# Kernel tuning notes

Hardware: AMD Instinct MI355X
Metric: run time of the kernel (lower is better)

The kernel has to match this reference:

```python
import jax, jax.numpy as jnp
import numpy as np

SEQ, BATCH, IN_F, STATE, OUT_F = 2048, 32, 256, 512, 256


def setup_inputs() -> dict:
    key = jax.random.key(0)
    k1, k2, k3, k4 = jax.random.split(key, 4)
    x = jax.random.normal(k1, (SEQ, BATCH, IN_F), dtype=jnp.float32)
    # lambda_log init per module __init__ with rmin=0, rmax=1:
    # u ~ U(0,1); lambda_log = log(-0.5*log(u*(rmax+rmin)*(rmax-rmin)+rmin^2)) = log(-0.5*log(u))
    u = jax.random.uniform(k2, (STATE,), dtype=jnp.float32, minval=1e-6, maxval=1.0)
    lambda_log = jnp.log(-0.5 * jnp.log(u))
    B = jax.random.normal(k3, (STATE, IN_F), dtype=jnp.float32) / np.float32(np.sqrt(IN_F))
    C = jax.random.normal(k4, (OUT_F, STATE), dtype=jnp.float32) / np.float32(np.sqrt(STATE))
    return {"input": x, "lambda_log": lambda_log, "B": B, "C": C}


def reference(input, lambda_log, B, C):
    # mode='sequential', inner_loops=1, rnn_burnin=0, done=None, hidden=None
    lamda = jnp.exp(-jnp.exp(lambda_log))                 # [N]
    gamma = jnp.sqrt(1.0 - lamda * lamda + 1e-7)          # [N]
    # project all timesteps at once: b_seq[s,b,n] = gamma_n * (x_s @ B^T)
    b_seq = jnp.einsum('sbi,ni->sbn', input, B) * gamma   # [S,B,N]

    def step(state, b_t):
        new_state = lamda * state + b_t                   # diagonal LRU recurrence
        return new_state, new_state

    init = jnp.zeros((input.shape[1], lambda_log.shape[0]), dtype=input.dtype)
    final_state, states = jax.lax.scan(step, init, b_seq)  # states: [S,B,N]
    output = jnp.einsum('sbn,on->sbo', states, C)          # [S,B,O]
    return output, final_state
```

## Files before the change

kernel.cpp:

```cpp
#include <hip/hip_runtime.h>

#define SEQ   2048
#define BATCH 32
#define INF   256
#define NST   512
#define OUTF  256
#define CLEN  32
#define NCH   64
#define NJOB  4
#define NCG   (NCH / NJOB)
#define NBLK  (NCG * BATCH)

typedef __bf16 bf16;
typedef __bf16 bf16x8 __attribute__((ext_vector_type(8)));
typedef float  f32x4  __attribute__((ext_vector_type(4)));
typedef unsigned long long ull;

__global__ void k_prep(const float* __restrict__ ll,
                       const float* __restrict__ Bm,
                       const float* __restrict__ Cm,
                       float* __restrict__ lam,
                       float* __restrict__ lamG,
                       float* __restrict__ l2la,
                       bf16* __restrict__ Bb,
                       bf16* __restrict__ Cb) {
  int i = blockIdx.x * 256 + threadIdx.x;
  if (i < NST) {
    float e = expf(ll[i]);
    float lmb = expf(-e);
    lam[i] = lmb;
    l2la[i] = -e * 1.44269504088896341f;
    float p = lmb;
#pragma unroll
    for (int q = 0; q < 7; ++q) p *= p;
    lamG[i] = p;
  }
  if (i < NST * INF) {
    int n = i >> 8;
    float lmb = expf(-expf(ll[n]));
    float g = sqrtf(1.0f - lmb * lmb + 1e-7f);
    Bb[i] = (bf16)(Bm[i] * g);
  }
  if (i < OUTF * NST) {
    Cb[i] = (bf16)(Cm[i]);
  }
}

__device__ __forceinline__ void xload(const float* __restrict__ xp, int tid,
                                      float4 xr[4]) {
#pragma unroll
  for (int rep = 0; rep < 4; ++rep) {
    int slot = rep * 512 + tid;
    int row = slot >> 6, col4 = slot & 63;
    xr[rep] = *(const float4*)(xp + (size_t)row * (BATCH * INF) + col4 * 4);
  }
}

__device__ __forceinline__ void xstore(char* xsb, int tid, const float4 xr[4]) {
#pragma unroll
  for (int rep = 0; rep < 4; ++rep) {
    int slot = rep * 512 + tid;
    int row = slot >> 6, col4 = slot & 63;
    union { bf16 h[4]; ull u; } pk;
    pk.h[0] = (bf16)xr[rep].x; pk.h[1] = (bf16)xr[rep].y;
    pk.h[2] = (bf16)xr[rep].z; pk.h[3] = (bf16)xr[rep].w;
    int byte = (row * (INF * 2) + col4 * 8) ^ ((row & 15) << 4);
    *(ull*)(xsb + byte) = pk.u;
  }
}

__device__ __forceinline__ void reg_scan(f32x4 acc[2][4], float carry[4],
                                         const float la[4], const float l4[4],
                                         int kg, int rl) {
#pragma unroll
  for (int mt = 0; mt < 2; ++mt) {
    float sl[4][4];
#pragma unroll
    for (int nt = 0; nt < 4; ++nt) {
      sl[nt][0] = acc[mt][nt][0];
      sl[nt][1] = fmaf(la[nt], sl[nt][0], acc[mt][nt][1]);
      sl[nt][2] = fmaf(la[nt], sl[nt][1], acc[mt][nt][2]);
      sl[nt][3] = fmaf(la[nt], sl[nt][2], acc[mt][nt][3]);
    }
    float G[4];
#pragma unroll
    for (int nt = 0; nt < 4; ++nt) {
      float g1 = __shfl_up(sl[nt][3], 16);
      G[nt] = (kg >= 1) ? fmaf(l4[nt], g1, sl[nt][3]) : sl[nt][3];
    }
#pragma unroll
    for (int nt = 0; nt < 4; ++nt) {
      float l8 = l4[nt] * l4[nt];
      float g2 = __shfl_up(G[nt], 32);
      G[nt] = (kg >= 2) ? fmaf(l8, g2, G[nt]) : G[nt];
    }
#pragma unroll
    for (int nt = 0; nt < 4; ++nt) {
      float X = __shfl_up(G[nt], 16);
      X = (kg >= 1) ? X : 0.0f;
      float l8 = l4[nt] * l4[nt];
      float p4k = ((kg & 1) ? l4[nt] : 1.0f) * ((kg & 2) ? l8 : 1.0f);
      float cin = fmaf(p4k, carry[nt], X);
      float l2 = la[nt] * la[nt], l3 = l2 * la[nt];
      acc[mt][nt][0] = fmaf(la[nt], cin, sl[nt][0]);
      acc[mt][nt][1] = fmaf(l2, cin, sl[nt][1]);
      acc[mt][nt][2] = fmaf(l3, cin, sl[nt][2]);
      acc[mt][nt][3] = fmaf(l4[nt], cin, sl[nt][3]);
    }
#pragma unroll
    for (int nt = 0; nt < 4; ++nt)
      carry[nt] = __shfl(acc[mt][nt][3], rl + 48);
  }
}

__device__ __forceinline__ void gemm1_l2(const char* xsb, const bf16* __restrict__ Bb,
                                         f32x4 acc[2][4], int n0, int rl, int kg) {
#pragma unroll
  for (int k = 0; k < 8; ++k) {
    bf16x8 af[2], bfr[4];
#pragma unroll
    for (int mt = 0; mt < 2; ++mt) {
      int row = mt * 16 + rl;
      int byte = (row * (INF * 2) + (k * 32 + kg * 8) * 2) ^ (rl << 4);
      af[mt] = *(const bf16x8*)(xsb + byte);
    }
#pragma unroll
    for (int nt = 0; nt < 4; ++nt)
      bfr[nt] = *(const bf16x8*)(Bb + (size_t)(n0 + nt * 16 + rl) * INF + k * 32 + kg * 8);
#pragma unroll
    for (int mt = 0; mt < 2; ++mt)
#pragma unroll
      for (int nt = 0; nt < 4; ++nt)
        acc[mt][nt] = __builtin_amdgcn_mfma_f32_16x16x32_bf16(af[mt], bfr[nt], acc[mt][nt], 0, 0, 0);
  }
}

__global__ __launch_bounds__(512, 2)
void k_pass0f(const float* __restrict__ x, const bf16* __restrict__ Bb,
              const float* __restrict__ lam, float* __restrict__ Z,
              ull* __restrict__ bfrag) {
  __shared__ __align__(16) char xs[4][CLEN * INF * 2];

  const int tid = threadIdx.x, wid = tid >> 6, lane = tid & 63;
  const int rl = lane & 15, kg = lane >> 4;
  const int b = blockIdx.x >> 4, cg = blockIdx.x & 15;
  const int n0 = wid * 64;

  float la[4], l4[4], carry[4];
#pragma unroll
  for (int nt = 0; nt < 4; ++nt) {
    float v = lam[n0 + nt * 16 + rl];
    la[nt] = v; l4[nt] = (v * v) * (v * v);
    carry[nt] = 0.0f;
  }

  bf16x8 Breg[8][4];
#pragma unroll
  for (int k = 0; k < 8; ++k)
#pragma unroll
    for (int nt = 0; nt < 4; ++nt)
      Breg[k][nt] = *(const bf16x8*)(Bb + (size_t)(n0 + nt * 16 + rl) * INF + k * 32 + kg * 8);

  {
    float4 xr[4];
    xload(x + ((size_t)(cg * NJOB * CLEN) * BATCH + b) * INF, tid, xr);
    xstore(xs[0], tid, xr);
    xload(x + ((size_t)((cg * NJOB + 1) * CLEN) * BATCH + b) * INF, tid, xr);
    xstore(xs[1], tid, xr);
  }
  __syncthreads();

#pragma unroll
  for (int jj = 0; jj < NJOB; ++jj) {
    const int c = cg * NJOB + jj;
    f32x4 acc[2][4] = {};
#pragma unroll
    for (int k = 0; k < 8; ++k) {
      bf16x8 af[2];
#pragma unroll
      for (int mt = 0; mt < 2; ++mt) {
        int row = mt * 16 + rl;
        int byte = (row * (INF * 2) + (k * 32 + kg * 8) * 2) ^ (rl << 4);
        af[mt] = *(const bf16x8*)(&xs[jj][0] + byte);
      }
#pragma unroll
      for (int mt = 0; mt < 2; ++mt)
#pragma unroll
        for (int nt = 0; nt < 4; ++nt)
          acc[mt][nt] = __builtin_amdgcn_mfma_f32_16x16x32_bf16(af[mt], Breg[k][nt], acc[mt][nt], 0, 0, 0);
    }

    float4 xr[4];
    if (jj < 2)
      xload(x + ((size_t)((c + 2) * CLEN) * BATCH + b) * INF, tid, xr);

    reg_scan(acc, carry, la, l4, kg, rl);

    if (jj < 2) {
      xstore(xs[jj + 2], tid, xr);
      __syncthreads();
    }

    {
      ull* dst = bfrag + ((size_t)(((cg * BATCH + b) * NJOB + jj) * 8 + wid)) * 512 + lane;
#pragma unroll
      for (int mt = 0; mt < 2; ++mt)
#pragma unroll
        for (int nt = 0; nt < 4; ++nt) {
          union { bf16 h[4]; ull u; } pk;
          pk.h[0] = (bf16)acc[mt][nt][0];
          pk.h[1] = (bf16)acc[mt][nt][1];
          pk.h[2] = (bf16)acc[mt][nt][2];
          pk.h[3] = (bf16)acc[mt][nt][3];
          dst[(mt * 4 + nt) * 64] = pk.u;
        }
    }

    if (jj == NJOB - 1) {
      if (kg == 0)
#pragma unroll
        for (int nt = 0; nt < 4; ++nt)
          Z[((size_t)cg * BATCH + b) * NST + n0 + nt * 16 + rl] = carry[nt];
    }
  }
}

__global__ __launch_bounds__(128)
void k_chain(const float* __restrict__ Z, const float* __restrict__ lamG,
             float* __restrict__ S0, float* __restrict__ fin) {
  const int b = blockIdx.x;
  const int n = blockIdx.y * 128 + threadIdx.x;
  const float lG = lamG[n];
  float z[NCG];
#pragma unroll
  for (int g = 0; g < NCG; ++g)
    z[g] = Z[((size_t)g * BATCH + b) * NST + n];
  float s = 0.0f;
#pragma unroll
  for (int g = 0; g < NCG; ++g) {
    S0[((size_t)g * BATCH + b) * NST + n] = s;
    s = fmaf(lG, s, z[g]);
  }
  fin[(size_t)b * NST + n] = s;
}

__global__ __launch_bounds__(512)
void k_gemm2d(const ull* __restrict__ bfrag, const bf16* __restrict__ Cb,
              const float* __restrict__ S0, const float* __restrict__ l2la,
              float* __restrict__ out) {
  __shared__ __align__(16) char ss[32 * NST * 2];

  const int tid = threadIdx.x, wid = tid >> 6, lane = tid & 63;
  const int rl = lane & 15, kg = lane >> 4;
  const int c = blockIdx.x >> 5, b = blockIdx.x & 31;
  const int cg = c >> 2, jj = c & 3;

  const ull* src8 = bfrag + ((size_t)((cg * BATCH + b) * NJOB + jj)) * 4096;
  const float* S0g = S0 + ((size_t)cg * BATCH + b) * NST;
#pragma unroll
  for (int q = 0; q < 8; ++q) {
    int chunk = q * 512 + tid;
    int widx = chunk >> 9;
    int fr = (chunk >> 6) & 7;
    int mt = fr >> 2, nt = fr & 3;
    int ls = chunk & 63;
    int kgs = ls >> 4, rls = ls & 15;
    int n = widx * 64 + nt * 16 + rls;
    int t0 = mt * 16 + kgs * 4;
    int dt0 = jj * 32 + t0;

    union { ull u; bf16 h[4]; } in;
    in.u = src8[chunk];
    float l2 = l2la[n];
    float s0 = S0g[n];
    float e = exp2f((float)(dt0 + 1) * l2);
    float lm = exp2f(l2);
#pragma unroll
    for (int r = 0; r < 4; ++r) {
      float s = fmaf(e, s0, (float)in.h[r]);
      int t = t0 + r;
      int byte = (t * (NST * 2) + n * 2) ^ ((t & 15) << 4);
      *(bf16*)(&ss[0] + byte) = (bf16)s;
      e *= lm;
    }
  }
  __syncthreads();

  const int o0 = wid * 32;
  f32x4 acc[2][2] = {};
  bf16x8 cf[2];
#pragma unroll
  for (int ot2 = 0; ot2 < 2; ++ot2)
    cf[ot2] = *(const bf16x8*)(Cb + (size_t)(o0 + ot2 * 16 + rl) * NST + kg * 8);
#pragma unroll
  for (int kq = 0; kq < 16; ++kq) {
    const int k0 = kq * 32;
    bf16x8 cfn[2];
    if (kq < 15)
#pragma unroll
      for (int ot2 = 0; ot2 < 2; ++ot2)
        cfn[ot2] = *(const bf16x8*)(Cb + (size_t)(o0 + ot2 * 16 + rl) * NST + k0 + 32 + kg * 8);
    bf16x8 af[2];
#pragma unroll
    for (int mf = 0; mf < 2; ++mf) {
      int t = mf * 16 + rl;
      af[mf] = *(const bf16x8*)(&ss[0] +
          ((t * (NST * 2) + (k0 + kg * 8) * 2) ^ ((t & 15) << 4)));
    }
#pragma unroll
    for (int mf = 0; mf < 2; ++mf)
#pragma unroll
      for (int ot2 = 0; ot2 < 2; ++ot2)
        acc[mf][ot2] = __builtin_amdgcn_mfma_f32_16x16x32_bf16(af[mf], cf[ot2], acc[mf][ot2], 0, 0, 0);
    if (kq < 15) {
      cf[0] = cfn[0]; cf[1] = cfn[1];
    }
  }

#pragma unroll
  for (int mf = 0; mf < 2; ++mf)
#pragma unroll
    for (int ot2 = 0; ot2 < 2; ++ot2)
#pragma unroll
      for (int r = 0; r < 4; ++r) {
        int ml = mf * 16 + kg * 4 + r;
        size_t srow = (size_t)c * 32 + ml;
        int o = o0 + ot2 * 16 + rl;
        out[(srow * BATCH + b) * OUTF + o] = acc[mf][ot2][r];
      }
}

__global__ __launch_bounds__(512, 2)
void k_pass0_fb(const float* __restrict__ x, const bf16* __restrict__ Bb,
                const float* __restrict__ lam, float* __restrict__ Z) {
  __shared__ __align__(16) char xs[2][CLEN * INF * 2];

  const int tid = threadIdx.x, wid = tid >> 6, lane = tid & 63;
  const int rl = lane & 15, kg = lane >> 4;
  const int b = blockIdx.x >> 4, cg = blockIdx.x & 15;
  const int n0 = wid * 64;

  float la[4], l4[4], carry[4];
#pragma unroll
  for (int nt = 0; nt < 4; ++nt) {
    float v = lam[n0 + nt * 16 + rl];
    la[nt] = v; l4[nt] = (v * v) * (v * v);
    carry[nt] = 0.0f;
  }

  bf16x8 Breg[8][4];
#pragma unroll
  for (int k = 0; k < 8; ++k)
#pragma unroll
    for (int nt = 0; nt < 4; ++nt)
      Breg[k][nt] = *(const bf16x8*)(Bb + (size_t)(n0 + nt * 16 + rl) * INF + k * 32 + kg * 8);

  {
    float4 xr0[4];
    xload(x + ((size_t)(cg * NJOB * CLEN) * BATCH + b) * INF, tid, xr0);
    xstore(xs[0], tid, xr0);
  }
  __syncthreads();

#pragma unroll
  for (int jj = 0; jj < NJOB; ++jj) {
    const int c = cg * NJOB + jj;
    f32x4 acc[2][4] = {};
#pragma unroll
    for (int k = 0; k < 8; ++k) {
      bf16x8 af[2];
#pragma unroll
      for (int mt = 0; mt < 2; ++mt) {
        int row = mt * 16 + rl;
        int byte = (row * (INF * 2) + (k * 32 + kg * 8) * 2) ^ (rl << 4);
        af[mt] = *(const bf16x8*)(&xs[jj & 1][0] + byte);
      }
#pragma unroll
      for (int mt = 0; mt < 2; ++mt)
#pragma unroll
        for (int nt = 0; nt < 4; ++nt)
          acc[mt][nt] = __builtin_amdgcn_mfma_f32_16x16x32_bf16(af[mt], Breg[k][nt], acc[mt][nt], 0, 0, 0);
    }

    if (jj < NJOB - 1) {
      float4 xr[4];
      xload(x + ((size_t)((c + 1) * CLEN) * BATCH + b) * INF, tid, xr);
      reg_scan(acc, carry, la, l4, kg, rl);
      xstore(xs[(jj + 1) & 1], tid, xr);
      __syncthreads();
    } else {
      reg_scan(acc, carry, la, l4, kg, rl);
      if (kg == 0)
#pragma unroll
        for (int nt = 0; nt < 4; ++nt)
          Z[((size_t)cg * BATCH + b) * NST + n0 + nt * 16 + rl] = carry[nt];
    }
  }
}

__global__ __launch_bounds__(512)
void k_pass1_fb(const float* __restrict__ x, const bf16* __restrict__ Bb,
                const bf16* __restrict__ Cb, const float* __restrict__ lam,
                const float* __restrict__ S0, float* __restrict__ out,
                float* __restrict__ fin) {
  __shared__ __align__(16) char xs[2][CLEN * INF * 2];
  __shared__ __align__(16) char ss[CLEN * NST * 2];

  const int tid = threadIdx.x, wid = tid >> 6, lane = tid & 63;
  const int rl = lane & 15, kg = lane >> 4;
  const int b = blockIdx.x >> 4, cg = blockIdx.x & 15;
  const int n0 = wid * 64;

  float la[4], l4[4], carry[4];
#pragma unroll
  for (int nt = 0; nt < 4; ++nt) {
    float v = lam[n0 + nt * 16 + rl];
    la[nt] = v; l4[nt] = (v * v) * (v * v);
    carry[nt] = S0[((size_t)cg * BATCH + b) * NST + n0 + nt * 16 + rl];
  }
  {
    float4 xr0[4];
    xload(x + ((size_t)(cg * NJOB * CLEN) * BATCH + b) * INF, tid, xr0);
    xstore(xs[0], tid, xr0);
  }
  __syncthreads();

#pragma unroll
  for (int jj = 0; jj < NJOB; ++jj) {
    const int c = cg * NJOB + jj;
    f32x4 acc[2][4] = {};
    gemm1_l2(&xs[jj & 1][0], Bb, acc, n0, rl, kg);
    {
      float4 xr[4];
      const int lastj = (jj == NJOB - 1);
      if (!lastj)
        xload(x + ((size_t)((c + 1) * CLEN) * BATCH + b) * INF, tid, xr);
      reg_scan(acc, carry, la, l4, kg, rl);
      if (c == NCH - 1 && kg == 0)
#pragma unroll
        for (int nt = 0; nt < 4; ++nt)
          fin[(size_t)b * NST + n0 + nt * 16 + rl] = carry[nt];
      __syncthreads();
#pragma unroll
      for (int mt = 0; mt < 2; ++mt)
#pragma unroll
        for (int nt = 0; nt < 4; ++nt)
#pragma unroll
          for (int r = 0; r < 4; ++r) {
            int t = mt * 16 + kg * 4 + r;
            int n = n0 + nt * 16 + rl;
            int byte = (t * (NST * 2) + n * 2) ^ ((t & 15) << 4);
            *(bf16*)(&ss[0] + byte) = (bf16)acc[mt][nt][r];
          }
      if (!lastj) xstore(xs[(jj + 1) & 1], tid, xr);
    }
    __syncthreads();

    const int o0 = wid * 32;
    f32x4 a2[2][2] = {};
#pragma unroll
    for (int k0 = 0; k0 < NST; k0 += 32) {
      bf16x8 af[2], cf[2];
#pragma unroll
      for (int mt = 0; mt < 2; ++mt) {
        int t = mt * 16 + rl;
        int byte = (t * (NST * 2) + (k0 + kg * 8) * 2) ^ (rl << 4);
        af[mt] = *(const bf16x8*)(&ss[0] + byte);
      }
#pragma unroll
      for (int ot = 0; ot < 2; ++ot)
        cf[ot] = *(const bf16x8*)(Cb + (size_t)(o0 + ot * 16 + rl) * NST + k0 + kg * 8);
#pragma unroll
      for (int mt = 0; mt < 2; ++mt)
#pragma unroll
        for (int ot = 0; ot < 2; ++ot)
          a2[mt][ot] = __builtin_amdgcn_mfma_f32_16x16x32_bf16(af[mt], cf[ot], a2[mt][ot], 0, 0, 0);
    }
#pragma unroll
    for (int mt = 0; mt < 2; ++mt)
#pragma unroll
      for (int ot = 0; ot < 2; ++ot)
#pragma unroll
        for (int r = 0; r < 4; ++r) {
          int t = mt * 16 + kg * 4 + r;
          int o = o0 + ot * 16 + rl;
          out[(((size_t)(c * CLEN + t)) * BATCH + b) * OUTF + o] = a2[mt][ot][r];
        }
  }
}

extern "C" void kernel_launch(void* const* d_in, const int* in_sizes, int n_in,
                              void* d_out, int out_size, void* d_ws, size_t ws_size,
                              hipStream_t stream) {
  const float* x  = (const float*)d_in[0];
  const float* ll = (const float*)d_in[1];
  const float* Bm = (const float*)d_in[2];
  const float* Cm = (const float*)d_in[3];

  char* ws = (char*)d_ws;
  float* lam  = (float*)(ws);
  float* lamG = (float*)(ws + 2048);
  float* l2la = (float*)(ws + 4096);
  bf16*  Bb   = (bf16*)(ws + 6144);
  bf16*  Cb   = (bf16*)(ws + 6144 + NST * INF * 2);
  float* Z    = (float*)(ws + 6144 + NST * INF * 2 + OUTF * NST * 2);
  float* S0   = (float*)((char*)Z + (size_t)NCG * BATCH * NST * 4);
  ull*   bfrag= (ull*)((char*)S0 + (size_t)NCG * BATCH * NST * 4);
  const size_t NEED = ((char*)bfrag - ws) + (size_t)SEQ * BATCH * NST * 2;

  float* out = (float*)d_out;
  float* fin = out + (size_t)SEQ * BATCH * OUTF;

  k_prep<<<dim3(512), dim3(256), 0, stream>>>(ll, Bm, Cm, lam, lamG, l2la, Bb, Cb);
  if (ws_size >= NEED) {
    k_pass0f<<<dim3(NBLK), dim3(512), 0, stream>>>(x, Bb, lam, Z, bfrag);
    k_chain<<<dim3(BATCH, 4), dim3(128), 0, stream>>>(Z, lamG, S0, fin);
    k_gemm2d<<<dim3(2048), dim3(512), 0, stream>>>(bfrag, Cb, S0, l2la, out);
  } else {
    k_pass0_fb<<<dim3(NBLK), dim3(512), 0, stream>>>(x, Bb, lam, Z);
    k_chain<<<dim3(BATCH, 4), dim3(128), 0, stream>>>(Z, lamG, S0, fin);
    k_pass1_fb<<<dim3(NBLK), dim3(512), 0, stream>>>(x, Bb, Cb, lam, S0, out, fin);
  }
}
```

Before: 121.2 us.

## Store intermediate scan in row-major layout and use precomputed lambda power table

The first pass now writes its bf16 intermediate states in a plain time-by-state row-major layout instead of MFMA fragment order, so the second GEMM kernel can load them with 16-byte vector reads. The per-element exp2 for the carry correction is replaced by a 128-row table of lambda powers built in the prep kernel. The GEMM kernel now handles 64 timesteps per block (half as many blocks) to get more reuse of the C fragments. The cost is scattered 2-byte stores in pass0, a serial 128-iteration loop in the prep kernel, extra table reads, and doubled shared memory per block.

```diff
diff --git a/kernel.cpp b/kernel.cpp
--- a/kernel.cpp
+++ b/kernel.cpp
@@ -21,7 +21,7 @@
                        const float* __restrict__ Cm,
                        float* __restrict__ lam,
                        float* __restrict__ lamG,
-                       float* __restrict__ l2la,
+                       float* __restrict__ Lam32,
                        bf16* __restrict__ Bb,
                        bf16* __restrict__ Cb) {
   int i = blockIdx.x * 256 + threadIdx.x;
@@ -29,11 +29,15 @@
     float e = expf(ll[i]);
     float lmb = expf(-e);
     lam[i] = lmb;
-    l2la[i] = -e * 1.44269504088896341f;
     float p = lmb;
 #pragma unroll
     for (int q = 0; q < 7; ++q) p *= p;
     lamG[i] = p;
+    float ee = lmb;
+    for (int dt = 0; dt < 128; ++dt) {
+      Lam32[(size_t)dt * NST + i] = ee;
+      ee *= lmb;
+    }
   }
   if (i < NST * INF) {
     int n = i >> 8;
@@ -136,9 +140,9 @@
 }
 
 __global__ __launch_bounds__(512, 2)
-void k_pass0f(const float* __restrict__ x, const bf16* __restrict__ Bb,
-              const float* __restrict__ lam, float* __restrict__ Z,
-              ull* __restrict__ bfrag) {
+void k_pass0tn(const float* __restrict__ x, const bf16* __restrict__ Bb,
+               const float* __restrict__ lam, float* __restrict__ Z,
+               bf16* __restrict__ bfrag) {
   __shared__ __align__(16) char xs[4][CLEN * INF * 2];
 
   const int tid = threadIdx.x, wid = tid >> 6, lane = tid & 63;
@@ -202,18 +206,17 @@
     }
 
     {
-      ull* dst = bfrag + ((size_t)(((cg * BATCH + b) * NJOB + jj) * 8 + wid)) * 512 + lane;
+      bf16* dstp = bfrag + (((size_t)cg * BATCH + b) * 128 + jj * 32) * NST;
 #pragma unroll
       for (int mt = 0; mt < 2; ++mt)
 #pragma unroll
-        for (int nt = 0; nt < 4; ++nt) {
-          union { bf16 h[4]; ull u; } pk;
-          pk.h[0] = (bf16)acc[mt][nt][0];
-          pk.h[1] = (bf16)acc[mt][nt][1];
-          pk.h[2] = (bf16)acc[mt][nt][2];
-          pk.h[3] = (bf16)acc[mt][nt][3];
-          dst[(mt * 4 + nt) * 64] = pk.u;
-        }
+        for (int nt = 0; nt < 4; ++nt)
+#pragma unroll
+          for (int r = 0; r < 4; ++r) {
+            int t = mt * 16 + kg * 4 + r;
+            int n = n0 + nt * 16 + rl;
+            dstp[(size_t)t * NST + n] = (bf16)acc[mt][nt][r];
+          }
     }
 
     if (jj == NJOB - 1) {
@@ -245,49 +248,46 @@
 }
 
 __global__ __launch_bounds__(512)
-void k_gemm2d(const ull* __restrict__ bfrag, const bf16* __restrict__ Cb,
-              const float* __restrict__ S0, const float* __restrict__ l2la,
+void k_gemm2e(const bf16* __restrict__ bfrag, const bf16* __restrict__ Cb,
+              const float* __restrict__ S0, const float* __restrict__ Lam32,
               float* __restrict__ out) {
-  __shared__ __align__(16) char ss[32 * NST * 2];
+  __shared__ __align__(16) char ss[64 * NST * 2];
 
   const int tid = threadIdx.x, wid = tid >> 6, lane = tid & 63;
   const int rl = lane & 15, kg = lane >> 4;
-  const int c = blockIdx.x >> 5, b = blockIdx.x & 31;
-  const int cg = c >> 2, jj = c & 3;
-
-  const ull* src8 = bfrag + ((size_t)((cg * BATCH + b) * NJOB + jj)) * 4096;
-  const float* S0g = S0 + ((size_t)cg * BATCH + b) * NST;
+  const int c2 = blockIdx.x >> 5, b = blockIdx.x & 31;
+  const int cg = c2 >> 1;
+  const int dtbase = (c2 & 1) * 64;
+
+  const int n8 = (tid & 63) * 8;
+  float s0g[8];
+#pragma unroll
+  for (int j = 0; j < 8; ++j)
+    s0g[j] = S0[((size_t)cg * BATCH + b) * NST + n8 + j];
+
+  const uint4* src = (const uint4*)(bfrag +
+      (((size_t)cg * BATCH + b) * 128 + dtbase) * NST);
 #pragma unroll
   for (int q = 0; q < 8; ++q) {
     int chunk = q * 512 + tid;
-    int widx = chunk >> 9;
-    int fr = (chunk >> 6) & 7;
-    int mt = fr >> 2, nt = fr & 3;
-    int ls = chunk & 63;
-    int kgs = ls >> 4, rls = ls & 15;
-    int n = widx * 64 + nt * 16 + rls;
-    int t0 = mt * 16 + kgs * 4;
-    int dt0 = jj * 32 + t0;
-
-    union { ull u; bf16 h[4]; } in;
-    in.u = src8[chunk];
-    float l2 = l2la[n];
-    float s0 = S0g[n];
-    float e = exp2f((float)(dt0 + 1) * l2);
-    float lm = exp2f(l2);
-#pragma unroll
-    for (int r = 0; r < 4; ++r) {
-      float s = fmaf(e, s0, (float)in.h[r]);
-      int t = t0 + r;
-      int byte = (t * (NST * 2) + n * 2) ^ ((t & 15) << 4);
-      *(bf16*)(&ss[0] + byte) = (bf16)s;
-      e *= lm;
-    }
+    int tl = chunk >> 6;
+    union { uint4 u; bf16 h[8]; } in, ot;
+    in.u = src[chunk];
+    const float4* lp = (const float4*)(Lam32 + (size_t)(dtbase + tl) * NST + n8);
+    float4 L0 = lp[0], L1 = lp[1];
+    float lv[8] = {L0.x, L0.y, L0.z, L0.w, L1.x, L1.y, L1.z, L1.w};
+#pragma unroll
+    for (int j = 0; j < 8; ++j) {
+      float s = fmaf(lv[j], s0g[j], (float)in.h[j]);
+      ot.h[j] = (bf16)s;
+    }
+    int byte = (tl * (NST * 2) + (chunk & 63) * 16) ^ ((tl & 15) << 4);
+    *(uint4*)(&ss[0] + byte) = ot.u;
   }
   __syncthreads();
 
   const int o0 = wid * 32;
-  f32x4 acc[2][2] = {};
+  f32x4 acc[4][2] = {};
   bf16x8 cf[2];
 #pragma unroll
   for (int ot2 = 0; ot2 < 2; ++ot2)
@@ -300,15 +300,15 @@
 #pragma unroll
       for (int ot2 = 0; ot2 < 2; ++ot2)
         cfn[ot2] = *(const bf16x8*)(Cb + (size_t)(o0 + ot2 * 16 + rl) * NST + k0 + 32 + kg * 8);
-    bf16x8 af[2];
-#pragma unroll
-    for (int mf = 0; mf < 2; ++mf) {
+    bf16x8 af[4];
+#pragma unroll
+    for (int mf = 0; mf < 4; ++mf) {
       int t = mf * 16 + rl;
       af[mf] = *(const bf16x8*)(&ss[0] +
           ((t * (NST * 2) + (k0 + kg * 8) * 2) ^ ((t & 15) << 4)));
     }
 #pragma unroll
-    for (int mf = 0; mf < 2; ++mf)
+    for (int mf = 0; mf < 4; ++mf)
 #pragma unroll
       for (int ot2 = 0; ot2 < 2; ++ot2)
         acc[mf][ot2] = __builtin_amdgcn_mfma_f32_16x16x32_bf16(af[mf], cf[ot2], acc[mf][ot2], 0, 0, 0);
@@ -318,13 +318,13 @@
   }
 
 #pragma unroll
-  for (int mf = 0; mf < 2; ++mf)
+  for (int mf = 0; mf < 4; ++mf)
 #pragma unroll
     for (int ot2 = 0; ot2 < 2; ++ot2)
 #pragma unroll
       for (int r = 0; r < 4; ++r) {
         int ml = mf * 16 + kg * 4 + r;
-        size_t srow = (size_t)c * 32 + ml;
+        size_t srow = (size_t)c2 * 64 + ml;
         int o = o0 + ot2 * 16 + rl;
         out[(srow * BATCH + b) * OUTF + o] = acc[mf][ot2][r];
       }
@@ -498,24 +498,24 @@
   const float* Cm = (const float*)d_in[3];
 
   char* ws = (char*)d_ws;
-  float* lam  = (float*)(ws);
-  float* lamG = (float*)(ws + 2048);
-  float* l2la = (float*)(ws + 4096);
-  bf16*  Bb   = (bf16*)(ws + 6144);
-  bf16*  Cb   = (bf16*)(ws + 6144 + NST * INF * 2);
-  float* Z    = (float*)(ws + 6144 + NST * INF * 2 + OUTF * NST * 2);
-  float* S0   = (float*)((char*)Z + (size_t)NCG * BATCH * NST * 4);
-  ull*   bfrag= (ull*)((char*)S0 + (size_t)NCG * BATCH * NST * 4);
+  float* lam   = (float*)(ws);
+  float* lamG  = (float*)(ws + 2048);
+  float* Lam32 = (float*)(ws + 4096);
+  bf16*  Bb    = (bf16*)(ws + 4096 + 262144);
+  bf16*  Cb    = (bf16*)((char*)Bb + (size_t)NST * INF * 2);
+  float* Z     = (float*)((char*)Cb + (size_t)OUTF * NST * 2);
+  float* S0    = (float*)((char*)Z + (size_t)NCG * BATCH * NST * 4);
+  bf16*  bfrag = (bf16*)((char*)S0 + (size_t)NCG * BATCH * NST * 4);
   const size_t NEED = ((char*)bfrag - ws) + (size_t)SEQ * BATCH * NST * 2;
 
   float* out = (float*)d_out;
   float* fin = out + (size_t)SEQ * BATCH * OUTF;
 
-  k_prep<<<dim3(512), dim3(256), 0, stream>>>(ll, Bm, Cm, lam, lamG, l2la, Bb, Cb);
+  k_prep<<<dim3(512), dim3(256), 0, stream>>>(ll, Bm, Cm, lam, lamG, Lam32, Bb, Cb);
   if (ws_size >= NEED) {
-    k_pass0f<<<dim3(NBLK), dim3(512), 0, stream>>>(x, Bb, lam, Z, bfrag);
+    k_pass0tn<<<dim3(NBLK), dim3(512), 0, stream>>>(x, Bb, lam, Z, bfrag);
     k_chain<<<dim3(BATCH, 4), dim3(128), 0, stream>>>(Z, lamG, S0, fin);
-    k_gemm2d<<<dim3(2048), dim3(512), 0, stream>>>(bfrag, Cb, S0, l2la, out);
+    k_gemm2e<<<dim3(1024), dim3(512), 0, stream>>>(bfrag, Cb, S0, Lam32, out);
   } else {
     k_pass0_fb<<<dim3(NBLK), dim3(512), 0, stream>>>(x, Bb, lam, Z);
     k_chain<<<dim3(BATCH, 4), dim3(128), 0, stream>>>(Z, lamG, S0, fin);
```

New measurement: 115.2 us. 5.0% less time.
